# Optimization experiments

Hardware: AMD Instinct MI355X
Metric: run time of the kernel (lower is better)

## Reference

```python
import jax, jax.numpy as jnp
import numpy as np

N = 100000
E = 1600000
IN, HID, OUT = 128, 64, 32


def setup_inputs() -> dict:
    key = jax.random.key(0)
    ks = jax.random.split(key, 8)
    x = jax.random.normal(ks[0], (N, IN), dtype=jnp.float32)
    edge_index = jax.random.randint(ks[1], (2, E), 0, N, dtype=jnp.int32)
    eps = jax.random.normal(ks[2], (N, OUT), dtype=jnp.float32)
    W1 = jax.random.normal(ks[3], (IN, HID), dtype=jnp.float32) / np.sqrt(IN)
    b1 = jnp.zeros((HID,), jnp.float32)
    Wmu = jax.random.normal(ks[4], (HID, OUT), dtype=jnp.float32) / np.sqrt(HID)
    bmu = jnp.zeros((OUT,), jnp.float32)
    Wls = jax.random.normal(ks[5], (HID, OUT), dtype=jnp.float32) / np.sqrt(HID)
    bls = jnp.zeros((OUT,), jnp.float32)
    return dict(x=x, edge_index=edge_index, eps=eps, W1=W1, b1=b1,
                Wmu=Wmu, bmu=bmu, Wls=Wls, bls=bls)


def reference(x, edge_index, eps, W1, b1, Wmu, bmu, Wls, bls):
    n = x.shape[0]
    src, dst = edge_index[0], edge_index[1]
    # GCN with self-loops and symmetric normalization (PyG GCNConv default)
    loop = jnp.arange(n, dtype=src.dtype)
    s = jnp.concatenate([src, loop])   # [E+N]
    d = jnp.concatenate([dst, loop])
    deg = jax.ops.segment_sum(jnp.ones_like(s, jnp.float32), d, num_segments=n)
    dis = jax.lax.rsqrt(jnp.maximum(deg, 1.0))  # deg >= 1 due to self-loops
    norm = dis[s] * dis[d]                       # [E+N]

    def gcn_conv(h, W, b):
        h = h @ W                                # transform first (small dim)
        msg = h[s] * norm[:, None]               # gather over edges
        return jax.ops.segment_sum(msg, d, num_segments=n) + b

    h = jax.nn.relu(gcn_conv(x, W1, b1))
    # F.normalize(h, p=2, dim=-1)
    h = h / jnp.maximum(jnp.linalg.norm(h, axis=-1, keepdims=True), 1e-12)
    mu = gcn_conv(h, Wmu, bmu)
    logstd = gcn_conv(h, Wls, bls)
    # reparametrize (training mode): mu + randn * exp(clamp(logstd, -10, 10))
    z = mu + eps * jnp.exp(jnp.clip(logstd, -10.0, 10.0))
    # decode: sigmoid(<z_i, z_j>) over original edges
    adj_pred = jax.nn.sigmoid(jnp.sum(z[src] * z[dst], axis=1))
    return adj_pred, mu, logstd
```

## Files before the change

kernel.cpp:

```cpp
#include <hip/hip_runtime.h>
#include <hip/hip_fp16.h>

#define NN 100000
#define NE 1600000
#define W_BKT 128
#define NB_BKT ((NN + W_BKT - 1) / W_BKT)
#define TILE_E 16384
#define NT ((NE + TILE_E - 1) / TILE_E)
#define STAGE_CAP 4352

typedef _Float16 half2v __attribute__((ext_vector_type(2)));
typedef _Float16 half4v __attribute__((ext_vector_type(4)));
typedef _Float16 half8v __attribute__((ext_vector_type(8)));
typedef float float2v __attribute__((ext_vector_type(2)));
typedef float float4v __attribute__((ext_vector_type(4)));


__global__ __launch_bounds__(256) void k_cnt(const int* __restrict__ dst,
                                             int* __restrict__ counts) {
    __shared__ int hc[NB_BKT];
    int tid = threadIdx.x;
    for (int i = tid; i < NB_BKT; i += 256) hc[i] = 0;
    __syncthreads();
    int base = blockIdx.x * TILE_E;
    int lim = base + TILE_E; if (lim > NE) lim = NE;
    for (int e = base + tid; e < lim; e += 256)
        atomicAdd(&hc[dst[e] >> 7], 1);
    __syncthreads();
    for (int i = tid; i < NB_BKT; i += 256)
        counts[blockIdx.x * NB_BKT + i] = hc[i];
}

__global__ __launch_bounds__(1024) void k_bscan(int* __restrict__ counts,
                                                int* __restrict__ bucket_base) {
    __shared__ int buf[1024];
    int tid = threadIdx.x;
    int total = 0;
    if (tid < NB_BKT)
        for (int t = 0; t < NT; ++t) total += counts[t * NB_BKT + tid];
    buf[tid] = total;
    __syncthreads();
    for (int off = 1; off < 1024; off <<= 1) {
        int v = (tid >= off) ? buf[tid - off] : 0;
        __syncthreads();
        buf[tid] += v;
        __syncthreads();
    }
    if (tid < NB_BKT) {
        int off = buf[tid] - total;
        bucket_base[tid] = off;
        for (int t = 0; t < NT; ++t) {
            int c = counts[t * NB_BKT + tid];
            counts[t * NB_BKT + tid] = off;
            off += c;
        }
    }
    if (tid == 0) bucket_base[NB_BKT] = NE;
}

__global__ __launch_bounds__(256) void k_place(const int* __restrict__ src,
                                               const int* __restrict__ dst,
                                               const int* __restrict__ counts,
                                               int* __restrict__ ebuf) {
    __shared__ int cur[NB_BKT];
    int tid = threadIdx.x;
    for (int i = tid; i < NB_BKT; i += 256)
        cur[i] = counts[blockIdx.x * NB_BKT + i];
    __syncthreads();
    int base = blockIdx.x * TILE_E;
    int lim = base + TILE_E; if (lim > NE) lim = NE;
    for (int e = base + tid; e < lim; e += 256) {
        int s = src[e], d = dst[e];
        int pos = atomicAdd(&cur[d >> 7], 1);
        ebuf[pos] = (s << 7) | (d & 127);
    }
}

__global__ __launch_bounds__(256) void k_build(const int* __restrict__ bucket_base,
                                               const int* __restrict__ ebuf,
                                               int* __restrict__ csr_src,
                                               int* __restrict__ row_ptr,
                                               float* __restrict__ dis) {
    __shared__ int deg[W_BKT];
    __shared__ int pre[W_BKT];
    __shared__ int cur[W_BKT];
    __shared__ int stage[STAGE_CAP];
    int b = blockIdx.x;
    int tid = threadIdx.x;
    int beg = bucket_base[b], end = bucket_base[b + 1];
    int n = end - beg;
    if (tid < W_BKT) deg[tid] = 0;
    __syncthreads();
    bool fits = (n <= STAGE_CAP);
    if (fits) {
        for (int i = tid; i < n; i += 256) {
            int val = ebuf[beg + i];
            stage[i] = val;
            atomicAdd(&deg[val & 127], 1);
        }
    } else {
        for (int i = tid; i < n; i += 256)
            atomicAdd(&deg[ebuf[beg + i] & 127], 1);
    }
    __syncthreads();
    if (tid < W_BKT) pre[tid] = deg[tid];
    __syncthreads();
    for (int off = 1; off < W_BKT; off <<= 1) {
        int v = (tid >= off && tid < W_BKT) ? pre[tid - off] : 0;
        __syncthreads();
        if (tid < W_BKT) pre[tid] += v;
        __syncthreads();
    }
    if (tid < W_BKT) {
        int v = b * W_BKT + tid;
        int rp = beg + pre[tid] - deg[tid];
        if (v < NN) {
            row_ptr[v] = rp;
            dis[v] = rsqrtf((float)(1 + deg[tid]));
        }
        cur[tid] = rp;
    }
    if (b == NB_BKT - 1 && tid == 0) row_ptr[NN] = NE;
    __syncthreads();
    if (fits) {
        for (int i = tid; i < n; i += 256) {
            int val = stage[i];
            int pos = atomicAdd(&cur[val & 127], 1);
            csr_src[pos] = val >> 7;
        }
    } else {
        for (int i = tid; i < n; i += 256) {
            int val = ebuf[beg + i];
            int pos = atomicAdd(&cur[val & 127], 1);
            csr_src[pos] = val >> 7;
        }
    }
}


__global__ __launch_bounds__(256) void k_wprep(const float* __restrict__ W1,
                                               const float* __restrict__ Wmu,
                                               const float* __restrict__ Wls,
                                               _Float16* __restrict__ wf1h,
                                               _Float16* __restrict__ wf1l,
                                               _Float16* __restrict__ wf2h,
                                               _Float16* __restrict__ wf2l) {
    int tid = threadIdx.x;
    for (int f = tid; f < 4 * 4 * 64; f += 256) {
        int lane = f & 63;
        int kc = (f >> 6) & 3;
        int ct = f >> 8;
        int col = ct * 16 + (lane & 15);
        int k0 = kc * 32 + (lane >> 4) * 8;
#pragma unroll
        for (int j = 0; j < 8; ++j) {
            float w = W1[(k0 + j) * 64 + col];
            _Float16 hi = (_Float16)w;
            wf1h[f * 8 + j] = hi;
            wf1l[f * 8 + j] = (_Float16)(w - (float)hi);
        }
    }
    for (int f = tid; f < 4 * 2 * 64; f += 256) {
        int lane = f & 63;
        int kc = (f >> 6) & 1;
        int ct = f >> 7;
        int col = ct * 16 + (lane & 15);
        int k0 = kc * 32 + (lane >> 4) * 8;
#pragma unroll
        for (int j = 0; j < 8; ++j) {
            int k = k0 + j;
            float w = (col < 32) ? Wmu[k * 32 + col] : Wls[k * 32 + (col - 32)];
            _Float16 hi = (_Float16)w;
            wf2h[f * 8 + j] = hi;
            wf2l[f * 8 + j] = (_Float16)(w - (float)hi);
        }
    }
}

__device__ __forceinline__ void split8(const float4 a, const float4 b,
                                       half8v& hi, half8v& lo) {
    float v[8] = {a.x, a.y, a.z, a.w, b.x, b.y, b.z, b.w};
#pragma unroll
    for (int i = 0; i < 8; ++i) {
        _Float16 h = (_Float16)v[i];
        hi[i] = h;
        lo[i] = (_Float16)(v[i] - (float)h);
    }
}

__global__ __launch_bounds__(256) void k_gemm1(const float* __restrict__ x,
                                               const _Float16* __restrict__ wf1h,
                                               const _Float16* __restrict__ wf1l,
                                               const float* __restrict__ dis,
                                               _Float16* __restrict__ t1) {
    int tid = threadIdx.x;
    int lane = tid & 63;
    int wv = tid >> 6;
    int wrow = blockIdx.x * 64 + wv * 16;
    int cl = lane & 15, kg = lane >> 4;
    const half8v* Bh = (const half8v*)wf1h;
    const half8v* Bl = (const half8v*)wf1l;
    float4v acc[4] = {};
    int r = wrow + cl;
    long rr = (r < NN) ? r : (NN - 1);
    const float4* xp = (const float4*)(x + rr * 128);
#pragma unroll
    for (int kc = 0; kc < 4; ++kc) {
        float4 xa = xp[kc * 8 + kg * 2];
        float4 xb = xp[kc * 8 + kg * 2 + 1];
        half8v ah, al;
        split8(xa, xb, ah, al);
#pragma unroll
        for (int ct = 0; ct < 4; ++ct) {
            half8v bh = Bh[(ct * 4 + kc) * 64 + lane];
            half8v bl = Bl[(ct * 4 + kc) * 64 + lane];
            acc[ct] = __builtin_amdgcn_mfma_f32_16x16x32_f16(ah, bh, acc[ct], 0, 0, 0);
            acc[ct] = __builtin_amdgcn_mfma_f32_16x16x32_f16(al, bh, acc[ct], 0, 0, 0);
            acc[ct] = __builtin_amdgcn_mfma_f32_16x16x32_f16(ah, bl, acc[ct], 0, 0, 0);
        }
    }
#pragma unroll
    for (int j = 0; j < 4; ++j) {
        int row = wrow + kg * 4 + j;
        if (row < NN) {
            float dv = dis[row];
#pragma unroll
            for (int ct = 0; ct < 4; ++ct)
                t1[(long)row * 64 + ct * 16 + cl] = (_Float16)(acc[ct][j] * dv);
        }
    }
}

__global__ __launch_bounds__(256) void k_gemm2(const _Float16* __restrict__ h,
                                               const _Float16* __restrict__ wf2h,
                                               const _Float16* __restrict__ wf2l,
                                               const float* __restrict__ dis,
                                               _Float16* __restrict__ t2) {
    int tid = threadIdx.x;
    int lane = tid & 63;
    int wv = tid >> 6;
    int wrow = blockIdx.x * 64 + wv * 16;
    int cl = lane & 15, kg = lane >> 4;
    const half8v* Bh = (const half8v*)wf2h;
    const half8v* Bl = (const half8v*)wf2l;
    float4v acc[4] = {};
    int r = wrow + cl;
    long rr = (r < NN) ? r : (NN - 1);
    const half8v* hp = (const half8v*)(h + rr * 64);
#pragma unroll
    for (int kc = 0; kc < 2; ++kc) {
        half8v ah = hp[kc * 4 + kg];
#pragma unroll
        for (int ct = 0; ct < 4; ++ct) {
            half8v bh = Bh[(ct * 2 + kc) * 64 + lane];
            half8v bl = Bl[(ct * 2 + kc) * 64 + lane];
            acc[ct] = __builtin_amdgcn_mfma_f32_16x16x32_f16(ah, bh, acc[ct], 0, 0, 0);
            acc[ct] = __builtin_amdgcn_mfma_f32_16x16x32_f16(ah, bl, acc[ct], 0, 0, 0);
        }
    }
#pragma unroll
    for (int j = 0; j < 4; ++j) {
        int row = wrow + kg * 4 + j;
        if (row < NN) {
            float dv = dis[row];
#pragma unroll
            for (int ct = 0; ct < 4; ++ct)
                t2[(long)row * 64 + ct * 16 + cl] = (_Float16)(acc[ct][j] * dv);
        }
    }
}


#define SWZ_LD(K) r[K] = t4[(__builtin_amdgcn_ds_swizzle(idx, ((K) << 5) | 0x10) << 4) + j4];

__device__ __forceinline__ void batch16_full(const half4v* __restrict__ t4, int idx,
                                             int j4, float* a) {
    half4v r[16];
    SWZ_LD(0)  SWZ_LD(1)  SWZ_LD(2)  SWZ_LD(3)
    SWZ_LD(4)  SWZ_LD(5)  SWZ_LD(6)  SWZ_LD(7)
    SWZ_LD(8)  SWZ_LD(9)  SWZ_LD(10) SWZ_LD(11)
    SWZ_LD(12) SWZ_LD(13) SWZ_LD(14) SWZ_LD(15)
#pragma unroll
    for (int k = 0; k < 16; ++k) {
        a[0] += (float)r[k][0]; a[1] += (float)r[k][1];
        a[2] += (float)r[k][2]; a[3] += (float)r[k][3];
    }
}

__device__ __forceinline__ void batch16_mask(const half4v* __restrict__ t4, int idx,
                                             int j4, int cnt, float* a) {
    half4v r[16];
    SWZ_LD(0)  SWZ_LD(1)  SWZ_LD(2)  SWZ_LD(3)
    SWZ_LD(4)  SWZ_LD(5)  SWZ_LD(6)  SWZ_LD(7)
    SWZ_LD(8)  SWZ_LD(9)  SWZ_LD(10) SWZ_LD(11)
    SWZ_LD(12) SWZ_LD(13) SWZ_LD(14) SWZ_LD(15)
#pragma unroll
    for (int k = 0; k < 16; ++k) {
        float w = (k < cnt) ? 1.0f : 0.0f;
        a[0] += w * (float)r[k][0]; a[1] += w * (float)r[k][1];
        a[2] += w * (float)r[k][2]; a[3] += w * (float)r[k][3];
    }
}

__device__ __forceinline__ void batch8_mask(const half4v* __restrict__ t4, int idx,
                                            int j4, int cnt, float* a) {
    half4v r[8];
    SWZ_LD(0)  SWZ_LD(1)  SWZ_LD(2)  SWZ_LD(3)
    SWZ_LD(4)  SWZ_LD(5)  SWZ_LD(6)  SWZ_LD(7)
#pragma unroll
    for (int k = 0; k < 8; ++k) {
        float w = (k < cnt) ? 1.0f : 0.0f;
        a[0] += w * (float)r[k][0]; a[1] += w * (float)r[k][1];
        a[2] += w * (float)r[k][2]; a[3] += w * (float)r[k][3];
    }
}

__global__ __launch_bounds__(512) void k_agg1(const half4v* __restrict__ tv4,
                                              const int* __restrict__ row_ptr,
                                              const int* __restrict__ csr_src,
                                              const float* __restrict__ dis,
                                              const float* __restrict__ b1,
                                              _Float16* __restrict__ h) {
    int lane = threadIdx.x & 63;
    int j4 = lane & 15;
    int v = blockIdx.x * 32 + (threadIdx.x >> 6) * 4 + (lane >> 4);
    int beg = row_ptr[v], end = row_ptr[v + 1];
    float a[4] = {0.f, 0.f, 0.f, 0.f};
    int base = beg;
    for (; base + 16 <= end; base += 16) {
        int idx = csr_src[base + j4];
        batch16_full(tv4, idx, j4, a);
    }
    int cnt = end - base;
    if (cnt > 0) {
        int idx = csr_src[base + ((j4 < cnt) ? j4 : cnt - 1)];
        if (cnt > 8) batch16_mask(tv4, idx, j4, cnt, a);
        else         batch8_mask(tv4, idx, j4, cnt, a);
    }
    float dv = dis[v];
    half4v rv = tv4[(v << 4) + j4];
    float4 bb = ((const float4*)b1)[j4];
    float val0 = fmaxf(dv * (a[0] + (float)rv[0]) + bb.x, 0.0f);
    float val1 = fmaxf(dv * (a[1] + (float)rv[1]) + bb.y, 0.0f);
    float val2 = fmaxf(dv * (a[2] + (float)rv[2]) + bb.z, 0.0f);
    float val3 = fmaxf(dv * (a[3] + (float)rv[3]) + bb.w, 0.0f);
    float ss = val0 * val0 + val1 * val1 + val2 * val2 + val3 * val3;
#pragma unroll
    for (int m = 1; m < 16; m <<= 1) ss += __shfl_xor(ss, m);
    float scale = 1.0f / fmaxf(sqrtf(ss), 1e-12f);
    half4v* h4 = (half4v*)h;
    half4v hv;
    hv[0] = (_Float16)(val0 * scale); hv[1] = (_Float16)(val1 * scale);
    hv[2] = (_Float16)(val2 * scale); hv[3] = (_Float16)(val3 * scale);
    h4[(v << 4) + j4] = hv;
}

__global__ __launch_bounds__(512) void k_agg2(const half4v* __restrict__ tv4,
                                              const int* __restrict__ row_ptr,
                                              const int* __restrict__ csr_src,
                                              const float* __restrict__ dis,
                                              const float* __restrict__ bmu,
                                              const float* __restrict__ bls,
                                              const float* __restrict__ eps,
                                              float* __restrict__ mu,
                                              float* __restrict__ ls,
                                              _Float16* __restrict__ zh) {
    int lane = threadIdx.x & 63;
    int j4 = lane & 15;
    int v = blockIdx.x * 32 + (threadIdx.x >> 6) * 4 + (lane >> 4);
    int beg = row_ptr[v], end = row_ptr[v + 1];
    float a[4] = {0.f, 0.f, 0.f, 0.f};
    int base = beg;
    for (; base + 16 <= end; base += 16) {
        int idx = csr_src[base + j4];
        batch16_full(tv4, idx, j4, a);
    }
    int cnt = end - base;
    if (cnt > 0) {
        int idx = csr_src[base + ((j4 < cnt) ? j4 : cnt - 1)];
        if (cnt > 8) batch16_mask(tv4, idx, j4, cnt, a);
        else         batch8_mask(tv4, idx, j4, cnt, a);
    }
    float dv = dis[v];
    half4v rv = tv4[(v << 4) + j4];
    float4 bb = (j4 < 8) ? ((const float4*)bmu)[j4] : ((const float4*)bls)[j4 - 8];
    float val0 = dv * (a[0] + (float)rv[0]) + bb.x;
    float val1 = dv * (a[1] + (float)rv[1]) + bb.y;
    float val2 = dv * (a[2] + (float)rv[2]) + bb.z;
    float val3 = dv * (a[3] + (float)rv[3]) + bb.w;
    float o0 = __shfl_xor(val0, 8);
    float o1 = __shfl_xor(val1, 8);
    float o2 = __shfl_xor(val2, 8);
    float o3 = __shfl_xor(val3, 8);
    float4v* mu4 = (float4v*)mu;
    float4v* ls4 = (float4v*)ls;
    half4v* z4  = (half4v*)zh;
    const float4* e4 = (const float4*)eps;
    if (j4 < 8) {
        float4v mv; mv.x = val0; mv.y = val1; mv.z = val2; mv.w = val3;
        __builtin_nontemporal_store(mv, &mu4[(v << 3) + j4]);
        float4 ev = e4[(v << 3) + j4];
        float l0 = fminf(fmaxf(o0, -10.0f), 10.0f);
        float l1 = fminf(fmaxf(o1, -10.0f), 10.0f);
        float l2 = fminf(fmaxf(o2, -10.0f), 10.0f);
        float l3 = fminf(fmaxf(o3, -10.0f), 10.0f);
        half4v zw;
        zw[0] = (_Float16)(val0 + ev.x * expf(l0));
        zw[1] = (_Float16)(val1 + ev.y * expf(l1));
        zw[2] = (_Float16)(val2 + ev.z * expf(l2));
        zw[3] = (_Float16)(val3 + ev.w * expf(l3));
        z4[(v << 3) + j4] = zw;
    } else {
        float4v lv; lv.x = val0; lv.y = val1; lv.z = val2; lv.w = val3;
        __builtin_nontemporal_store(lv, &ls4[(v << 3) + (j4 - 8)]);
    }
}

__global__ __launch_bounds__(256) void k_decode(const _Float16* __restrict__ zh,
                                                const int* __restrict__ src,
                                                const int* __restrict__ dst,
                                                float* __restrict__ out) {
    long t = (long)blockIdx.x * 256 + threadIdx.x;
    long e = t >> 2; int l = (int)(t & 3);
    if (e >= NE) return;
    int s = src[e], d = dst[e];
    const half8v* z8 = (const half8v*)zh;
    half8v a = z8[s * 4 + l];
    half8v b = z8[d * 4 + l];
    float p = 0.f;
#pragma unroll
    for (int i = 0; i < 8; ++i) p += (float)a[i] * (float)b[i];
    p += __shfl_xor(p, 1);
    p += __shfl_xor(p, 2);
    if (l == 0) out[e] = 1.0f / (1.0f + expf(-p));
}

extern "C" void kernel_launch(void* const* d_in, const int* in_sizes, int n_in,
                              void* d_out, int out_size, void* d_ws, size_t ws_size,
                              hipStream_t stream) {
    const float* x   = (const float*)d_in[0];
    const int*   ei  = (const int*)d_in[1];
    const float* eps = (const float*)d_in[2];
    const float* W1  = (const float*)d_in[3];
    const float* b1  = (const float*)d_in[4];
    const float* Wmu = (const float*)d_in[5];
    const float* bmu = (const float*)d_in[6];
    const float* Wls = (const float*)d_in[7];
    const float* bls = (const float*)d_in[8];
    const int* src = ei;
    const int* dst = ei + NE;

    float* out = (float*)d_out;
    float* adj = out;
    float* mu  = out + NE;
    float* ls  = mu + (long)NN * 32;

    float* dis      = (float*)d_ws;
    int*   row_ptr  = (int*)(dis + NN);
    int*   bucket_base = row_ptr + 100004;
    int*   counts   = bucket_base + 784;
    int*   ebuf     = counts + 76640;
    int*   csr_src  = ebuf + NE;
    _Float16* t     = (_Float16*)(csr_src + NE);
    _Float16* h     = t + (long)NN * 64;
    _Float16* zh    = h + (long)NN * 64 + 24;

    _Float16* wf1h = (_Float16*)counts;
    _Float16* wf1l = wf1h + 8192;
    _Float16* wf2h = wf1l + 8192;
    _Float16* wf2l = wf2h + 4096;

    const int B = 256;

    k_cnt  <<<NT, B, 0, stream>>>(dst, counts);
    k_bscan<<<1, 1024, 0, stream>>>(counts, bucket_base);
    k_place<<<NT, B, 0, stream>>>(src, dst, counts, ebuf);
    k_wprep<<<1, B, 0, stream>>>(W1, Wmu, Wls, wf1h, wf1l, wf2h, wf2l);
    k_build<<<NB_BKT, B, 0, stream>>>(bucket_base, ebuf, csr_src, row_ptr, dis);

    k_gemm1<<<(NN + 63) / 64, B, 0, stream>>>(x, wf1h, wf1l, dis, t);
    k_agg1 <<<NN / 32, 512, 0, stream>>>((const half4v*)t, row_ptr, csr_src, dis, b1, h);

    k_gemm2<<<(NN + 63) / 64, B, 0, stream>>>(h, wf2h, wf2l, dis, t);
    k_agg2 <<<NN / 32, 512, 0, stream>>>((const half4v*)t, row_ptr, csr_src, dis,
                                         bmu, bls, eps, mu, ls, zh);

    k_decode<<<(int)(((long)NE * 4 + B - 1) / B), B, 0, stream>>>(zh, src, dst, adj);
}
```

Baseline: 359.2 us.

## Decode edges per destination bucket with z tile staged in LDS

The decode kernel now walks the dst-bucketed edge buffer, one block per 128-node bucket. It loads that bucket's z rows into shared memory, so only the source row is gathered from global memory, and it scatters each result to its original edge slot through a new eid array written in k_place. The aggregation kernels also move from 512-thread to 256-thread blocks. The trade is an extra 1.6M-int write and read for eid plus scattered output stores, in exchange for halving the random z gathers.

```diff
diff --git a/kernel.cpp b/kernel.cpp
--- a/kernel.cpp
+++ b/kernel.cpp
@@ -61,7 +61,8 @@
 __global__ __launch_bounds__(256) void k_place(const int* __restrict__ src,
                                                const int* __restrict__ dst,
                                                const int* __restrict__ counts,
-                                               int* __restrict__ ebuf) {
+                                               int* __restrict__ ebuf,
+                                               int* __restrict__ eid) {
     __shared__ int cur[NB_BKT];
     int tid = threadIdx.x;
     for (int i = tid; i < NB_BKT; i += 256)
@@ -73,6 +74,7 @@
         int s = src[e], d = dst[e];
         int pos = atomicAdd(&cur[d >> 7], 1);
         ebuf[pos] = (s << 7) | (d & 127);
+        eid[pos] = e;
     }
 }
 
@@ -315,7 +317,7 @@
     }
 }
 
-__global__ __launch_bounds__(512) void k_agg1(const half4v* __restrict__ tv4,
+__global__ __launch_bounds__(256) void k_agg1(const half4v* __restrict__ tv4,
                                               const int* __restrict__ row_ptr,
                                               const int* __restrict__ csr_src,
                                               const float* __restrict__ dis,
@@ -323,7 +325,7 @@
                                               _Float16* __restrict__ h) {
     int lane = threadIdx.x & 63;
     int j4 = lane & 15;
-    int v = blockIdx.x * 32 + (threadIdx.x >> 6) * 4 + (lane >> 4);
+    int v = blockIdx.x * 16 + (threadIdx.x >> 6) * 4 + (lane >> 4);
     int beg = row_ptr[v], end = row_ptr[v + 1];
     float a[4] = {0.f, 0.f, 0.f, 0.f};
     int base = beg;
@@ -355,7 +357,7 @@
     h4[(v << 4) + j4] = hv;
 }
 
-__global__ __launch_bounds__(512) void k_agg2(const half4v* __restrict__ tv4,
+__global__ __launch_bounds__(256) void k_agg2(const half4v* __restrict__ tv4,
                                               const int* __restrict__ row_ptr,
                                               const int* __restrict__ csr_src,
                                               const float* __restrict__ dis,
@@ -367,7 +369,7 @@
                                               _Float16* __restrict__ zh) {
     int lane = threadIdx.x & 63;
     int j4 = lane & 15;
-    int v = blockIdx.x * 32 + (threadIdx.x >> 6) * 4 + (lane >> 4);
+    int v = blockIdx.x * 16 + (threadIdx.x >> 6) * 4 + (lane >> 4);
     int beg = row_ptr[v], end = row_ptr[v + 1];
     float a[4] = {0.f, 0.f, 0.f, 0.f};
     int base = beg;
@@ -417,22 +419,42 @@
 }
 
 __global__ __launch_bounds__(256) void k_decode(const _Float16* __restrict__ zh,
-                                                const int* __restrict__ src,
-                                                const int* __restrict__ dst,
+                                                const int* __restrict__ bucket_base,
+                                                const int* __restrict__ ebuf,
+                                                const int* __restrict__ eid,
                                                 float* __restrict__ out) {
-    long t = (long)blockIdx.x * 256 + threadIdx.x;
-    long e = t >> 2; int l = (int)(t & 3);
-    if (e >= NE) return;
-    int s = src[e], d = dst[e];
-    const half8v* z8 = (const half8v*)zh;
-    half8v a = z8[s * 4 + l];
-    half8v b = z8[d * 4 + l];
-    float p = 0.f;
-#pragma unroll
-    for (int i = 0; i < 8; ++i) p += (float)a[i] * (float)b[i];
-    p += __shfl_xor(p, 1);
-    p += __shfl_xor(p, 2);
-    if (l == 0) out[e] = 1.0f / (1.0f + expf(-p));
+    __shared__ _Float16 zl[W_BKT * 32];
+    int b = blockIdx.x;
+    int tid = threadIdx.x;
+    int base_node = b * W_BKT;
+    int nrows = NN - base_node; if (nrows > W_BKT) nrows = W_BKT;
+    {
+        const float4* zsrc = (const float4*)(zh + (long)base_node * 32);
+        float4* zdst = (float4*)zl;
+        for (int i = tid; i < nrows * 4; i += 256) zdst[i] = zsrc[i];
+    }
+    __syncthreads();
+    int beg = bucket_base[b], end = bucket_base[b + 1];
+    int lane = tid & 63;
+    int g = lane >> 3, j = lane & 7;
+    int wv = tid >> 6;
+    const half4v* z4 = (const half4v*)zh;
+    const half4v* zl4 = (const half4v*)zl;
+    for (int base = beg + wv * 8; base < end; base += 32) {
+        int cnt = end - base; if (cnt > 8) cnt = 8;
+        int p = base + ((g < cnt) ? g : cnt - 1);
+        int val = ebuf[p];
+        int s = val >> 7, dloc = val & 127;
+        half4v za = z4[((long)s << 3) + j];
+        half4v zv = zl4[(dloc << 3) + j];
+        float d = (float)za[0] * (float)zv[0] + (float)za[1] * (float)zv[1] +
+                  (float)za[2] * (float)zv[2] + (float)za[3] * (float)zv[3];
+        d += __shfl_xor(d, 1);
+        d += __shfl_xor(d, 2);
+        d += __shfl_xor(d, 4);
+        if (j == 0 && g < cnt)
+            out[eid[p]] = 1.0f / (1.0f + expf(-d));
+    }
 }
 
 extern "C" void kernel_launch(void* const* d_in, const int* in_sizes, int n_in,
@@ -461,7 +483,8 @@
     int*   counts   = bucket_base + 784;
     int*   ebuf     = counts + 76640;
     int*   csr_src  = ebuf + NE;
-    _Float16* t     = (_Float16*)(csr_src + NE);
+    int*   eid      = csr_src + NE;
+    _Float16* t     = (_Float16*)(eid + NE);
     _Float16* h     = t + (long)NN * 64;
     _Float16* zh    = h + (long)NN * 64 + 24;
 
@@ -474,16 +497,16 @@
 
     k_cnt  <<<NT, B, 0, stream>>>(dst, counts);
     k_bscan<<<1, 1024, 0, stream>>>(counts, bucket_base);
-    k_place<<<NT, B, 0, stream>>>(src, dst, counts, ebuf);
+    k_place<<<NT, B, 0, stream>>>(src, dst, counts, ebuf, eid);
     k_wprep<<<1, B, 0, stream>>>(W1, Wmu, Wls, wf1h, wf1l, wf2h, wf2l);
     k_build<<<NB_BKT, B, 0, stream>>>(bucket_base, ebuf, csr_src, row_ptr, dis);
 
     k_gemm1<<<(NN + 63) / 64, B, 0, stream>>>(x, wf1h, wf1l, dis, t);
-    k_agg1 <<<NN / 32, 512, 0, stream>>>((const half4v*)t, row_ptr, csr_src, dis, b1, h);
+    k_agg1 <<<NN / 16, B, 0, stream>>>((const half4v*)t, row_ptr, csr_src, dis, b1, h);
 
     k_gemm2<<<(NN + 63) / 64, B, 0, stream>>>(h, wf2h, wf2l, dis, t);
-    k_agg2 <<<NN / 32, 512, 0, stream>>>((const half4v*)t, row_ptr, csr_src, dis,
-                                         bmu, bls, eps, mu, ls, zh);
-
-    k_decode<<<(int)(((long)NE * 4 + B - 1) / B), B, 0, stream>>>(zh, src, dst, adj);
-}
+    k_agg2 <<<NN / 16, B, 0, stream>>>((const half4v*)t, row_ptr, csr_src, dis,
+                                       bmu, bls, eps, mu, ls, zh);
+
+    k_decode<<<NB_BKT, B, 0, stream>>>(zh, bucket_base, ebuf, eid, adj);
+}
```

New measurement: 439.4 us. 1.22x slower.
